# Optimization experiments

Measured on AMD Instinct MI355X. Metric: run time of the kernel, lower is better.

The kernel has to match this reference:

```python
import jax, jax.numpy as jnp
import numpy as np

N, E, D, H, L = 10000, 80000, 1024, 8, 2
C = D // H          # 128 per-head channels
NEG = 0.2           # GATv2 default negative_slope


def setup_inputs() -> dict:
    k = jax.random.split(jax.random.key(0), 16)
    s = 0.02
    return {
        "x": jax.random.normal(k[0], (N, D), jnp.float32),
        "edge_index": jax.random.randint(k[1], (2, E), 0, N),
        "edge_attr": jax.random.randint(k[2], (E,), 0, 3),
        "node_types": jax.random.randint(k[3], (N,), 0, 5),
        "node_type_emb": s * jax.random.normal(k[4], (5, D), jnp.float32),
        "edge_type_emb": s * jax.random.normal(k[5], (3, D), jnp.float32),
        "Wl": s * jax.random.normal(k[6], (L, D, D), jnp.float32),
        "bl": jnp.zeros((L, D), jnp.float32),
        "Wr": s * jax.random.normal(k[7], (L, D, D), jnp.float32),
        "br": jnp.zeros((L, D), jnp.float32),
        "We": s * jax.random.normal(k[8], (L, D, D), jnp.float32),
        "att": s * jax.random.normal(k[9], (L, H, C), jnp.float32),
        "conv_bias": jnp.zeros((L, D), jnp.float32),
        "out_W": s * jax.random.normal(k[10], (D, D), jnp.float32),
        "out_b": jnp.zeros((D,), jnp.float32),
    }


def _gatv2(h, src, dst, ee, Wl, bl, Wr, br, We, att, b):
    """PyG GATv2Conv: concat=True, add_self_loops=True (fill_value='mean')."""
    n = h.shape[0]
    xl = (h @ Wl + bl).reshape(n, H, C)   # source transform (lin_l)
    xr = (h @ Wr + br).reshape(n, H, C)   # target transform (lin_r)
    # self loops: edge_attr of a loop = mean of raw incoming edge feats
    cnt = jax.ops.segment_sum(jnp.ones(src.shape, jnp.float32), dst, num_segments=n)
    loop_attr = jax.ops.segment_sum(ee, dst, num_segments=n) / jnp.maximum(cnt, 1.0)[:, None]
    loops = jnp.arange(n)
    s2 = jnp.concatenate([src, loops])
    d2 = jnp.concatenate([dst, loops])
    ea = jnp.concatenate([ee, loop_attr], axis=0)          # [E+N, D]
    ep = (ea @ We).reshape(-1, H, C)                        # lin_edge (no bias)
    e = jax.nn.leaky_relu(xl[s2] + xr[d2] + ep, NEG)        # [E+N, H, C]
    logit = jnp.einsum('ehc,hc->eh', e, att)                # attention logits
    # segment softmax over destination nodes (every node has a self loop)
    m = jax.ops.segment_max(logit, d2, num_segments=n)
    a = jnp.exp(logit - m[d2])
    alpha = a / jax.ops.segment_sum(a, d2, num_segments=n)[d2]
    out = jax.ops.segment_sum(alpha[:, :, None] * xl[s2], d2, num_segments=n)
    return out.reshape(n, D) + b


def reference(x, edge_index, edge_attr, node_types, node_type_emb, edge_type_emb,
              Wl, bl, Wr, br, We, att, conv_bias, out_W, out_b):
    h = x + node_type_emb[node_types]
    ee = edge_type_emb[edge_attr]
    src, dst = edge_index[0], edge_index[1]
    for i in range(L):  # num_layers = 2
        h = h + jax.nn.relu(_gatv2(h, src, dst, ee, Wl[i], bl[i], Wr[i], br[i],
                                   We[i], att[i], conv_bias[i]))
    return h @ out_W + out_b
```

## Files before the change

kernel.cpp:

```cpp
#include <hip/hip_runtime.h>
#include <hip/hip_bf16.h>
#include <stdint.h>

typedef __bf16 bf16_t;
typedef bf16_t bf16x8 __attribute__((ext_vector_type(8)));
typedef bf16_t bf16x4 __attribute__((ext_vector_type(4)));
typedef float f32x4 __attribute__((ext_vector_type(4)));

#define NN 10000
#define EE 80000
#define DD 1024
#define LL 2
#define MPAD 10112
#define NEGS 0.2f

#define GLOAD_LDS16(g, l) \
    __builtin_amdgcn_global_load_lds((__attribute__((address_space(1))) void*)(void*)(g), \
                                     (__attribute__((address_space(3))) void*)(l), 16, 0, 0)

__global__ __launch_bounds__(256)
void preamble(const float* __restrict__ Wl, const float* __restrict__ Wr,
              const float* __restrict__ outW, bf16_t* __restrict__ WT,
              bf16_t* __restrict__ OWT,
              const float* __restrict__ x, const int* __restrict__ ntypes,
              const float* __restrict__ nte, bf16_t* __restrict__ hbuf,
              const float* __restrict__ bl, const float* __restrict__ br,
              const float* __restrict__ outb, float* __restrict__ biasb,
              float* __restrict__ M3L, int* __restrict__ deg)
{
    __shared__ float tile[32][33];
    int b = blockIdx.x;
    int tid = threadIdx.x;
    if (b < 5120) {
        int z = b >> 10, rem = b & 1023;
        int bx = rem & 31, by = rem >> 5;
        const float* src;
        bf16_t* dstp;
        switch (z) {
            case 0: src = Wl;                       dstp = WT;                        break;
            case 1: src = Wr;                       dstp = WT + (size_t)1024*1024;    break;
            case 2: src = Wl + (size_t)1024*1024;   dstp = WT + (size_t)2*1024*1024;  break;
            case 3: src = Wr + (size_t)1024*1024;   dstp = WT + (size_t)3*1024*1024;  break;
            default: src = outW;                    dstp = OWT;                       break;
        }
        int tx = tid & 31, ty = tid >> 5;
#pragma unroll
        for (int i = 0; i < 4; ++i)
            tile[ty + i*8][tx] = src[(size_t)(by*32 + ty + i*8)*1024 + bx*32 + tx];
        __syncthreads();
#pragma unroll
        for (int i = 0; i < 4; ++i)
            dstp[(size_t)(bx*32 + ty + i*8)*1024 + by*32 + tx] = (bf16_t)tile[tx][ty + i*8];
    } else if (b < 10176) {
        size_t idx = ((size_t)(b - 5120)*256 + tid) * 8;
        if (idx >= (size_t)MPAD*1024) return;
        int n = (int)(idx >> 10);
        int c = (int)(idx & 1023);
        bf16x8 outv;
        if (n < NN) {
            const float* xp = x + (size_t)n*1024 + c;
            int t = ntypes[n];
            const float* ep = nte + (size_t)t*1024 + c;
#pragma unroll
            for (int j = 0; j < 8; ++j) outv[j] = (bf16_t)(xp[j] + ep[j]);
        } else {
#pragma unroll
            for (int j = 0; j < 8; ++j) outv[j] = (bf16_t)0.f;
        }
        *(bf16x8*)(hbuf + idx) = outv;
    } else if (b < 10196) {
        int i = (b - 10176)*256 + tid;
        if (i < 4096) {
            int l = i >> 11, j = i & 2047;
            biasb[i] = (j < 1024) ? bl[l*1024 + j] : br[l*1024 + j - 1024];
        } else if (i < 5120) {
            biasb[i] = outb[i - 4096];
        }
    } else if (b < 10220) {
        int i = (b - 10196)*256 + tid;
        if (i < LL*3072) M3L[i] = 0.f;
    } else {
        int i = (b - 10220)*256 + tid;
        if (i < NN) deg[i] = 0;
    }
}

__global__ __launch_bounds__(256)
void compute_m3_all(const float* __restrict__ ete, const float* __restrict__ We,
                    float* __restrict__ M3L)
{
    int l   = blockIdx.x >> 8;
    int bid = blockIdx.x & 255;
    const float* WeL = We + (size_t)l*1024*1024;
    float* M3 = M3L + l*3072;
    int j  = (bid & 3) * 256 + threadIdx.x;
    int k0 = (bid >> 2) * 16;
    float a0 = 0.f, a1 = 0.f, a2 = 0.f;
#pragma unroll
    for (int kk = 0; kk < 16; ++kk) {
        int k = k0 + kk;
        float w = WeL[(size_t)k*1024 + j];
        a0 += ete[k]        * w;
        a1 += ete[1024 + k] * w;
        a2 += ete[2048 + k] * w;
    }
    atomicAdd(&M3[j],        a0);
    atomicAdd(&M3[1024 + j], a1);
    atomicAdd(&M3[2048 + j], a2);
}

__global__ void hist_k(const int* __restrict__ dsts, int* __restrict__ deg)
{ int e = blockIdx.x*256 + threadIdx.x; if (e < EE) atomicAdd(&deg[dsts[e]], 1); }

__global__ __launch_bounds__(1024)
void scan_csr(const int* __restrict__ deg, int* __restrict__ rp, int* __restrict__ cursor)
{
    __shared__ int tot[1024];
    int t = threadIdx.x;
    int base = t * 10;
    int v[10];
    int run = 0;
#pragma unroll
    for (int j = 0; j < 10; ++j) {
        int i = base + j;
        int d = (i < NN) ? deg[i] : 0;
        run += d;
        v[j] = run;
    }
    tot[t] = run;
    __syncthreads();
    for (int d = 1; d < 1024; d <<= 1) {
        int xv = (t >= d) ? tot[t - d] : 0;
        __syncthreads();
        tot[t] += xv;
        __syncthreads();
    }
    int ex = (t == 0) ? 0 : tot[t - 1];
#pragma unroll
    for (int j = 0; j < 10; ++j) {
        int i = base + j;
        if (i < NN) {
            int incl = ex + v[j];
            rp[i + 1] = incl;
            if (i + 1 < NN) cursor[i + 1] = incl;
        }
    }
    if (t == 0) { rp[0] = 0; cursor[0] = 0; }
}

__global__ void fill_csr(const int* __restrict__ srcs, const int* __restrict__ dsts,
                         const int* __restrict__ etype, int* __restrict__ cursor,
                         int* __restrict__ sorted_src, int* __restrict__ sorted_typ)
{
    int e = blockIdx.x*256 + threadIdx.x;
    if (e < EE) {
        int d = dsts[e];
        int pos = atomicAdd(&cursor[d], 1);
        sorted_src[pos] = srcs[e];
        sorted_typ[pos] = etype[e];
    }
}

template <typename OT>
__global__ __launch_bounds__(256)
void gemm_bt(const bf16_t* __restrict__ A, const bf16_t* __restrict__ BT,
             const float* __restrict__ bias, OT* __restrict__ Cmat,
             int K, int Ntot, int storeM, int mtiles, int ntiles)
{
    __shared__ __align__(16) bf16_t As[128*64];
    __shared__ __align__(16) bf16_t Bs[128*64];
    const int tid  = threadIdx.x;
    const int wave = tid >> 6;
    const int lane = tid & 63;

    const int GROUP_M = 8;
    int pid = blockIdx.x;
    int in_group = GROUP_M * ntiles;
    int gid = pid / in_group;
    int first_m = gid * GROUP_M;
    int gsz = mtiles - first_m; if (gsz > GROUP_M) gsz = GROUP_M;
    int local = pid % in_group;
    const int m0 = (first_m + (local % gsz)) * 128;
    const int n0 = (local / gsz) * 128;

    const int wm = (wave & 1) * 64;
    const int wn = (wave >> 1) * 64;
    const int quad = lane >> 4;
    const int l16  = lane & 15;

    const int srow = lane >> 3;
    const int gcol = ((lane & 7) ^ srow) * 8;

    f32x4 acc[4][4];
    f32x4 zero = {0.f, 0.f, 0.f, 0.f};
#pragma unroll
    for (int i = 0; i < 4; ++i)
#pragma unroll
        for (int j = 0; j < 4; ++j) acc[i][j] = zero;

    const bf16_t* aBase = A  + (size_t)(m0 + wave*8 + srow) * K + gcol;
    const bf16_t* bBase = BT + (size_t)(n0 + wave*8 + srow) * K + gcol;
    bf16_t* asDst = As + wave*512;
    bf16_t* bsDst = Bs + wave*512;

    for (int k0 = 0; k0 < K; k0 += 64) {
#pragma unroll
        for (int j = 0; j < 4; ++j)
            GLOAD_LDS16(aBase + (size_t)(j*32)*K + k0, asDst + j*2048);
#pragma unroll
        for (int j = 0; j < 4; ++j)
            GLOAD_LDS16(bBase + (size_t)(j*32)*K + k0, bsDst + j*2048);
        __syncthreads();
#pragma unroll
        for (int kk = 0; kk < 2; ++kk) {
            bf16x8 af[4], bfr[4];
#pragma unroll
            for (int mi = 0; mi < 4; ++mi) {
                int row = wm + mi*16 + l16;
                int ch  = ((kk*4 + quad) ^ (row & 7)) * 8;
                af[mi] = *(const bf16x8*)(As + row*64 + ch);
            }
#pragma unroll
            for (int ni = 0; ni < 4; ++ni) {
                int row = wn + ni*16 + l16;
                int ch  = ((kk*4 + quad) ^ (row & 7)) * 8;
                bfr[ni] = *(const bf16x8*)(Bs + row*64 + ch);
            }
#pragma unroll
            for (int mi = 0; mi < 4; ++mi)
#pragma unroll
                for (int ni = 0; ni < 4; ++ni)
                    acc[mi][ni] = __builtin_amdgcn_mfma_f32_16x16x32_bf16(af[mi], bfr[ni], acc[mi][ni], 0, 0, 0);
        }
        __syncthreads();
    }

#pragma unroll
    for (int mi = 0; mi < 4; ++mi) {
#pragma unroll
        for (int ni = 0; ni < 4; ++ni) {
            int col = n0 + wn + ni*16 + l16;
            float bv = bias[col];
#pragma unroll
            for (int r = 0; r < 4; ++r) {
                int row = m0 + wm + mi*16 + quad*4 + r;
                if (row < storeM)
                    Cmat[(size_t)row * Ntot + col] = (OT)(acc[mi][ni][r] + bv);
            }
        }
    }
}

__global__ __launch_bounds__(256)
void fused_edge(const int* __restrict__ rp, const int* __restrict__ ssrc,
                const int* __restrict__ styp, const bf16_t* __restrict__ XLXR,
                const float* __restrict__ M3, const float* __restrict__ attv,
                const float* __restrict__ cbias, bf16_t* __restrict__ hbuf)
{
    __shared__ float s_m3[3072];
    __shared__ float s_p[256*8];
    __shared__ int s_src[256];
    __shared__ int s_typ[256];
    __shared__ int s_cnt[3];

    int node = blockIdx.x;
    int tid = threadIdx.x;
    int lane = tid & 63;
    int wave = tid >> 6;

    for (int i = tid; i < 3072; i += 256) s_m3[i] = M3[i];
    if (tid < 3) s_cnt[tid] = 0;

    int b = rp[node], en = rp[node + 1];

    int c16 = lane * 16;
    bf16x8 xra = *(const bf16x8*)(XLXR + (size_t)node*2048 + 1024 + c16);
    bf16x8 xrb = *(const bf16x8*)(XLXR + (size_t)node*2048 + 1024 + c16 + 8);
    float xr16[16], at16[16];
#pragma unroll
    for (int j = 0; j < 8; ++j) { xr16[j] = (float)xra[j]; xr16[8+j] = (float)xrb[j]; }
#pragma unroll
    for (int j = 0; j < 16; ++j) at16[j] = attv[c16 + j];

    int c = tid * 4;
    int head = tid >> 5;
    bf16x4 xlv = *(const bf16x4*)(XLXR + (size_t)node*2048 + c);
    bf16x4 xrv = *(const bf16x4*)(XLXR + (size_t)node*2048 + 1024 + c);
    float at0 = attv[c], at1 = attv[c+1], at2 = attv[c+2], at3 = attv[c+3];

    float a0 = 0.f, a1 = 0.f, a2 = 0.f, a3 = 0.f;
    float den = 0.f;

    for (int base = b; base < en; base += 256) {
        int nchunk = en - base; if (nchunk > 256) nchunk = 256;
        __syncthreads();
        if (tid < nchunk) { s_src[tid] = ssrc[base + tid]; s_typ[tid] = styp[base + tid]; }
        __syncthreads();
        for (int i = wave; i < nchunk; i += 4) {
            int s = s_src[i];
            int t = s_typ[i];
            bf16x8 xa = *(const bf16x8*)(XLXR + (size_t)s*2048 + c16);
            bf16x8 xb = *(const bf16x8*)(XLXR + (size_t)s*2048 + c16 + 8);
            const float* m3p = s_m3 + t*1024 + c16;
            float part = 0.f;
#pragma unroll
            for (int j = 0; j < 8; ++j) {
                float v = (float)xa[j] + xr16[j] + m3p[j];
                v = (v > 0.f) ? v : NEGS * v;
                part += v * at16[j];
            }
#pragma unroll
            for (int j = 0; j < 8; ++j) {
                float v = (float)xb[j] + xr16[8+j] + m3p[8+j];
                v = (v > 0.f) ? v : NEGS * v;
                part += v * at16[8+j];
            }
            part += __shfl_xor(part, 1);
            part += __shfl_xor(part, 2);
            part += __shfl_xor(part, 4);
            if ((lane & 7) == 0) {
                part = fminf(fmaxf(part, -60.f), 60.f);
                s_p[i*8 + (lane >> 3)] = __expf(part);
            }
            if (lane == 0) atomicAdd(&s_cnt[t], 1);
        }
        __syncthreads();
#pragma unroll 2
        for (int i = 0; i < nchunk; ++i) {
            float p = s_p[i*8 + head];
            bf16x4 xs = *(const bf16x4*)(XLXR + (size_t)s_src[i]*2048 + c);
            den += p;
            a0 += p*(float)xs[0]; a1 += p*(float)xs[1];
            a2 += p*(float)xs[2]; a3 += p*(float)xs[3];
        }
    }
    __syncthreads();

    float cnt0 = (float)s_cnt[0], cnt1 = (float)s_cnt[1], cnt2 = (float)s_cnt[2];
    float degf = cnt0 + cnt1 + cnt2;
    float inv = 1.f / fmaxf(degf, 1.f);
    float w0 = cnt0 * inv, w1 = cnt1 * inv, w2 = cnt2 * inv;
    float sx0 = (float)xlv[0], sx1 = (float)xlv[1], sx2 = (float)xlv[2], sx3 = (float)xlv[3];
    float xr0 = (float)xrv[0], xr1 = (float)xrv[1], xr2 = (float)xrv[2], xr3 = (float)xrv[3];
    float e0 = w0*s_m3[c+0] + w1*s_m3[1024+c+0] + w2*s_m3[2048+c+0];
    float e1 = w0*s_m3[c+1] + w1*s_m3[1024+c+1] + w2*s_m3[2048+c+1];
    float e2 = w0*s_m3[c+2] + w1*s_m3[1024+c+2] + w2*s_m3[2048+c+2];
    float e3 = w0*s_m3[c+3] + w1*s_m3[1024+c+3] + w2*s_m3[2048+c+3];
    float u0 = sx0 + xr0 + e0; u0 = (u0 > 0.f) ? u0 : NEGS * u0;
    float u1 = sx1 + xr1 + e1; u1 = (u1 > 0.f) ? u1 : NEGS * u1;
    float u2 = sx2 + xr2 + e2; u2 = (u2 > 0.f) ? u2 : NEGS * u2;
    float u3 = sx3 + xr3 + e3; u3 = (u3 > 0.f) ? u3 : NEGS * u3;
    float sp = u0*at0 + u1*at1 + u2*at2 + u3*at3;
    sp += __shfl_xor(sp, 1);
    sp += __shfl_xor(sp, 2);
    sp += __shfl_xor(sp, 4);
    sp += __shfl_xor(sp, 8);
    sp += __shfl_xor(sp, 16);
    sp = fminf(fmaxf(sp, -60.f), 60.f);
    float ps = __expf(sp);
    den += ps;
    a0 += ps * sx0; a1 += ps * sx1; a2 += ps * sx2; a3 += ps * sx3;

    float invd = 1.f / den;
    bf16x4 hv = *(const bf16x4*)(hbuf + (size_t)node*1024 + c);
    const float* cb = cbias + c;
    bf16x4 outv;
    outv[0] = (bf16_t)((float)hv[0] + fmaxf(a0*invd + cb[0], 0.f));
    outv[1] = (bf16_t)((float)hv[1] + fmaxf(a1*invd + cb[1], 0.f));
    outv[2] = (bf16_t)((float)hv[2] + fmaxf(a2*invd + cb[2], 0.f));
    outv[3] = (bf16_t)((float)hv[3] + fmaxf(a3*invd + cb[3], 0.f));
    *(bf16x4*)(hbuf + (size_t)node*1024 + c) = outv;
}

extern "C" void kernel_launch(void* const* d_in, const int* in_sizes, int n_in,
                              void* d_out, int out_size, void* d_ws, size_t ws_size,
                              hipStream_t stream)
{
    (void)in_sizes; (void)n_in; (void)out_size; (void)ws_size;
    const float* x     = (const float*)d_in[0];
    const int*   eidx  = (const int*)d_in[1];
    const int*   etype = (const int*)d_in[2];
    const int*   ntyp  = (const int*)d_in[3];
    const float* nte   = (const float*)d_in[4];
    const float* ete   = (const float*)d_in[5];
    const float* Wl    = (const float*)d_in[6];
    const float* bl    = (const float*)d_in[7];
    const float* Wr    = (const float*)d_in[8];
    const float* br    = (const float*)d_in[9];
    const float* We    = (const float*)d_in[10];
    const float* attw  = (const float*)d_in[11];
    const float* cbias = (const float*)d_in[12];
    const float* outW  = (const float*)d_in[13];
    const float* outb  = (const float*)d_in[14];
    const int* srcs = eidx;
    const int* dsts = eidx + EE;

    char* wsp = (char*)d_ws;
    size_t off = 0;
    auto carve = [&](size_t bytes) -> void* {
        void* pp = wsp + off;
        off += (bytes + 255) & ~(size_t)255;
        return pp;
    };
    bf16_t* hbuf  = (bf16_t*)carve((size_t)MPAD*1024*2);
    bf16_t* XLXR  = (bf16_t*)carve((size_t)MPAD*2048*2);
    bf16_t* WT    = (bf16_t*)carve((size_t)LL*2048*1024*2);
    bf16_t* OWT   = (bf16_t*)carve((size_t)1024*1024*2);
    float*  M3L   = (float*)carve((size_t)LL*3072*4);
    float*  biasb = (float*)carve(5120*4);
    int* deg    = (int*)carve((size_t)NN*4);
    int* rp     = (int*)carve((size_t)(NN+1)*4);
    int* cursor = (int*)carve((size_t)NN*4);
    int* ssrc   = (int*)carve((size_t)EE*4);
    int* styp   = (int*)carve((size_t)EE*4);

    preamble<<<10260, 256, 0, stream>>>(Wl, Wr, outW, WT, OWT,
                                        x, ntyp, nte, hbuf,
                                        bl, br, outb, biasb, M3L, deg);
    compute_m3_all<<<512, 256, 0, stream>>>(ete, We, M3L);
    hist_k<<<(EE + 255)/256, 256, 0, stream>>>(dsts, deg);
    scan_csr<<<1, 1024, 0, stream>>>(deg, rp, cursor);
    fill_csr<<<(EE + 255)/256, 256, 0, stream>>>(srcs, dsts, etype, cursor, ssrc, styp);

    for (int l = 0; l < LL; ++l) {
        gemm_bt<bf16_t><<<79*16, 256, 0, stream>>>(hbuf, WT + (size_t)l*2048*1024,
                                                   biasb + l*2048, XLXR,
                                                   1024, 2048, MPAD, 79, 16);
        fused_edge<<<NN, 256, 0, stream>>>(rp, ssrc, styp, XLXR, M3L + l*3072, attw + l*1024,
                                           cbias + l*1024, hbuf);
    }

    gemm_bt<float><<<79*8, 256, 0, stream>>>(hbuf, OWT, biasb + 4096, (float*)d_out,
                                             1024, 1024, NN, 79, 8);
}
```

Baseline: 475.7 us.

## Fuse edge logit and aggregation into a single pass per thread

The edge kernel previously ran two passes per chunk. In the first, each wave computed edge logits over 16 channels per lane and stored them in shared memory. In the second, the whole block re-gathered the source features to aggregate. Now every thread handles its 4 channels of every edge in one pass: it computes the logit with a 32-lane shuffle reduction, exponentiates, and accumulates immediately. This removes the second gather of source rows, the shared logit buffer, the LDS copy of the edge-type table (now held in registers) and the shared atomics for type counts. The trade-off is that each of the 4 waves now redundantly does the full reduction and exp work for every edge, instead of one wave handling a quarter of the edges.

```diff
diff --git a/kernel.cpp b/kernel.cpp
--- a/kernel.cpp
+++ b/kernel.cpp
@@ -257,95 +257,67 @@
                 const float* __restrict__ M3, const float* __restrict__ attv,
                 const float* __restrict__ cbias, bf16_t* __restrict__ hbuf)
 {
-    __shared__ float s_m3[3072];
-    __shared__ float s_p[256*8];
+    int node = blockIdx.x;
+    int tid = threadIdx.x;
+    int c = tid * 4;
     __shared__ int s_src[256];
     __shared__ int s_typ[256];
-    __shared__ int s_cnt[3];
-
-    int node = blockIdx.x;
-    int tid = threadIdx.x;
-    int lane = tid & 63;
-    int wave = tid >> 6;
-
-    for (int i = tid; i < 3072; i += 256) s_m3[i] = M3[i];
-    if (tid < 3) s_cnt[tid] = 0;
 
     int b = rp[node], en = rp[node + 1];
 
-    int c16 = lane * 16;
-    bf16x8 xra = *(const bf16x8*)(XLXR + (size_t)node*2048 + 1024 + c16);
-    bf16x8 xrb = *(const bf16x8*)(XLXR + (size_t)node*2048 + 1024 + c16 + 8);
-    float xr16[16], at16[16];
-#pragma unroll
-    for (int j = 0; j < 8; ++j) { xr16[j] = (float)xra[j]; xr16[8+j] = (float)xrb[j]; }
-#pragma unroll
-    for (int j = 0; j < 16; ++j) at16[j] = attv[c16 + j];
-
-    int c = tid * 4;
-    int head = tid >> 5;
     bf16x4 xlv = *(const bf16x4*)(XLXR + (size_t)node*2048 + c);
     bf16x4 xrv = *(const bf16x4*)(XLXR + (size_t)node*2048 + 1024 + c);
+    float xr0 = (float)xrv[0], xr1 = (float)xrv[1], xr2 = (float)xrv[2], xr3 = (float)xrv[3];
     float at0 = attv[c], at1 = attv[c+1], at2 = attv[c+2], at3 = attv[c+3];
+    float m3r[3][4];
+#pragma unroll
+    for (int t = 0; t < 3; ++t)
+#pragma unroll
+        for (int j = 0; j < 4; ++j) m3r[t][j] = M3[t*1024 + c + j];
 
     float a0 = 0.f, a1 = 0.f, a2 = 0.f, a3 = 0.f;
     float den = 0.f;
+    float cnt0 = 0.f, cnt1 = 0.f, cnt2 = 0.f;
 
     for (int base = b; base < en; base += 256) {
         int nchunk = en - base; if (nchunk > 256) nchunk = 256;
         __syncthreads();
         if (tid < nchunk) { s_src[tid] = ssrc[base + tid]; s_typ[tid] = styp[base + tid]; }
         __syncthreads();
-        for (int i = wave; i < nchunk; i += 4) {
+#pragma unroll 2
+        for (int i = 0; i < nchunk; ++i) {
             int s = s_src[i];
             int t = s_typ[i];
-            bf16x8 xa = *(const bf16x8*)(XLXR + (size_t)s*2048 + c16);
-            bf16x8 xb = *(const bf16x8*)(XLXR + (size_t)s*2048 + c16 + 8);
-            const float* m3p = s_m3 + t*1024 + c16;
-            float part = 0.f;
-#pragma unroll
-            for (int j = 0; j < 8; ++j) {
-                float v = (float)xa[j] + xr16[j] + m3p[j];
-                v = (v > 0.f) ? v : NEGS * v;
-                part += v * at16[j];
-            }
-#pragma unroll
-            for (int j = 0; j < 8; ++j) {
-                float v = (float)xb[j] + xr16[8+j] + m3p[8+j];
-                v = (v > 0.f) ? v : NEGS * v;
-                part += v * at16[8+j];
-            }
+            bf16x4 xs = *(const bf16x4*)(XLXR + (size_t)s*2048 + c);
+            float x0 = (float)xs[0], x1 = (float)xs[1], x2 = (float)xs[2], x3 = (float)xs[3];
+            float v0 = x0 + xr0 + m3r[t][0]; v0 = (v0 > 0.f) ? v0 : NEGS * v0;
+            float v1 = x1 + xr1 + m3r[t][1]; v1 = (v1 > 0.f) ? v1 : NEGS * v1;
+            float v2 = x2 + xr2 + m3r[t][2]; v2 = (v2 > 0.f) ? v2 : NEGS * v2;
+            float v3 = x3 + xr3 + m3r[t][3]; v3 = (v3 > 0.f) ? v3 : NEGS * v3;
+            float part = v0*at0 + v1*at1 + v2*at2 + v3*at3;
             part += __shfl_xor(part, 1);
             part += __shfl_xor(part, 2);
             part += __shfl_xor(part, 4);
-            if ((lane & 7) == 0) {
-                part = fminf(fmaxf(part, -60.f), 60.f);
-                s_p[i*8 + (lane >> 3)] = __expf(part);
-            }
-            if (lane == 0) atomicAdd(&s_cnt[t], 1);
-        }
-        __syncthreads();
-#pragma unroll 2
-        for (int i = 0; i < nchunk; ++i) {
-            float p = s_p[i*8 + head];
-            bf16x4 xs = *(const bf16x4*)(XLXR + (size_t)s_src[i]*2048 + c);
+            part += __shfl_xor(part, 8);
+            part += __shfl_xor(part, 16);
+            part = fminf(fmaxf(part, -60.f), 60.f);
+            float p = __expf(part);
+            cnt0 += (t == 0) ? 1.f : 0.f;
+            cnt1 += (t == 1) ? 1.f : 0.f;
+            cnt2 += (t == 2) ? 1.f : 0.f;
             den += p;
-            a0 += p*(float)xs[0]; a1 += p*(float)xs[1];
-            a2 += p*(float)xs[2]; a3 += p*(float)xs[3];
-        }
-    }
-    __syncthreads();
-
-    float cnt0 = (float)s_cnt[0], cnt1 = (float)s_cnt[1], cnt2 = (float)s_cnt[2];
-    float degf = cnt0 + cnt1 + cnt2;
-    float inv = 1.f / fmaxf(degf, 1.f);
+            a0 += p * x0; a1 += p * x1; a2 += p * x2; a3 += p * x3;
+        }
+    }
+
+    float deg = cnt0 + cnt1 + cnt2;
+    float inv = 1.f / fmaxf(deg, 1.f);
     float w0 = cnt0 * inv, w1 = cnt1 * inv, w2 = cnt2 * inv;
     float sx0 = (float)xlv[0], sx1 = (float)xlv[1], sx2 = (float)xlv[2], sx3 = (float)xlv[3];
-    float xr0 = (float)xrv[0], xr1 = (float)xrv[1], xr2 = (float)xrv[2], xr3 = (float)xrv[3];
-    float e0 = w0*s_m3[c+0] + w1*s_m3[1024+c+0] + w2*s_m3[2048+c+0];
-    float e1 = w0*s_m3[c+1] + w1*s_m3[1024+c+1] + w2*s_m3[2048+c+1];
-    float e2 = w0*s_m3[c+2] + w1*s_m3[1024+c+2] + w2*s_m3[2048+c+2];
-    float e3 = w0*s_m3[c+3] + w1*s_m3[1024+c+3] + w2*s_m3[2048+c+3];
+    float e0 = w0*m3r[0][0] + w1*m3r[1][0] + w2*m3r[2][0];
+    float e1 = w0*m3r[0][1] + w1*m3r[1][1] + w2*m3r[2][1];
+    float e2 = w0*m3r[0][2] + w1*m3r[1][2] + w2*m3r[2][2];
+    float e3 = w0*m3r[0][3] + w1*m3r[1][3] + w2*m3r[2][3];
     float u0 = sx0 + xr0 + e0; u0 = (u0 > 0.f) ? u0 : NEGS * u0;
     float u1 = sx1 + xr1 + e1; u1 = (u1 > 0.f) ? u1 : NEGS * u1;
     float u2 = sx2 + xr2 + e2; u2 = (u2 > 0.f) ? u2 : NEGS * u2;
```

Result: faster. 404.0 us (-15.1%).
